# Kernel optimization log

Measured on AMD Instinct MI355X. Metric: run time of the kernel, lower is better.

## Reference

```python
import jax, jax.numpy as jnp
import numpy as np

N_NODES = 20000
N_EDGES = 320000
N_GRAPHS = 100
NEG_SLOPE = 0.2  # DGL GATConv default


def _gat_layer(x, src, dst, W, al, ar, b):
    # x: [N, Din]; W: [Din, H*D]; al, ar: [H, D]; b: [H*D]
    H, D = al.shape
    N = x.shape[0]
    f = (x @ W).reshape(N, H, D)                      # projected feats [N,H,D]
    el = (f * al[None]).sum(-1)                       # [N,H]
    er = (f * ar[None]).sum(-1)                       # [N,H]
    e = jax.nn.leaky_relu(el[src] + er[dst], NEG_SLOPE)  # [E,H] edge logits
    m = jax.ops.segment_max(e, dst, num_segments=N)   # per-dst max for stability
    m = jnp.where(jnp.isfinite(m), m, 0.0)            # zero-in-degree safety
    ex = jnp.exp(e - m[dst])                          # [E,H]
    s = jax.ops.segment_sum(ex, dst, num_segments=N)  # [N,H]
    a = ex / s[dst]                                   # edge softmax
    msg = f[src] * a[:, :, None]                      # [E,H,D]
    out = jax.ops.segment_sum(msg, dst, num_segments=N)  # [N,H,D]
    return out + b.reshape(1, H, D)


def setup_inputs() -> dict:
    key = jax.random.key(0)
    ks = jax.random.split(key, 16)
    x = jax.random.normal(ks[0], (N_NODES, 64), jnp.float32)
    src = jax.random.randint(ks[1], (N_EDGES,), 0, N_NODES, jnp.int32)
    dst = jax.random.randint(ks[2], (N_EDGES,), 0, N_NODES, jnp.int32)
    graph_id = jnp.sort(jax.random.randint(ks[3], (N_NODES,), 0, N_GRAPHS, jnp.int32))
    sc = lambda k, s: jax.random.normal(k, s, jnp.float32) * (1.0 / np.sqrt(s[0]))
    return {
        'x': x, 'src': src, 'dst': dst, 'graph_id': graph_id,
        'W1': sc(ks[4], (64, 640)), 'al1': jax.random.normal(ks[5], (10, 64)) * 0.1,
        'ar1': jax.random.normal(ks[6], (10, 64)) * 0.1, 'b1': jnp.zeros((640,), jnp.float32),
        'W2': sc(ks[7], (64, 128)), 'al2': jax.random.normal(ks[8], (1, 128)) * 0.1,
        'ar2': jax.random.normal(ks[9], (1, 128)) * 0.1, 'b2': jnp.zeros((128,), jnp.float32),
        'lw1': sc(ks[10], (128, 128)), 'lb1': jnp.zeros((128,), jnp.float32),
        'lw2': sc(ks[11], (128, 1)), 'lb2': jnp.zeros((1,), jnp.float32),
    }


def reference(x, src, dst, graph_id, W1, al1, ar1, b1, W2, al2, ar2, b2, lw1, lb1, lw2, lb2):
    h = jax.nn.relu(_gat_layer(x, src, dst, W1, al1, ar1, b1))   # [N,10,64]
    h = h.sum(axis=1)                                            # [N,64]
    h = jax.nn.relu(_gat_layer(h, src, dst, W2, al2, ar2, b2))   # [N,1,128]
    g = jax.ops.segment_max(h, graph_id, num_segments=N_GRAPHS)  # [B,1,128] max readout
    g = jnp.where(jnp.isfinite(g), g, 0.0)                       # empty-graph safety
    g = jax.nn.relu(g @ lw1 + lb1)                               # [B,1,128]
    g = jax.nn.relu(g @ lw2 + lb2)                               # [B,1,1]
    return g.reshape(-1)                                         # [B]
```

## Files before the change

### kernel.cpp

```cpp
#include <hip/hip_runtime.h>
#include <hip/hip_fp16.h>
#include <math.h>

typedef _Float16 half8 __attribute__((ext_vector_type(8)));
typedef float floatx4 __attribute__((ext_vector_type(4)));

__device__ __forceinline__ float leaky(float v){ return v > 0.f ? v : 0.2f*v; }

__device__ __forceinline__ float wredsum(float v){
  #pragma unroll
  for (int o=32;o>0;o>>=1) v += __shfl_xor(v,o,64);
  return v;
}

__device__ __forceinline__ unsigned fkey(float f){
  unsigned b = __float_as_uint(f);
  return (b & 0x80000000u) ? ~b : (b | 0x80000000u);
}
__device__ __forceinline__ float funkey(unsigned u){
  unsigned b = (u & 0x80000000u) ? (u ^ 0x80000000u) : ~u;
  return __uint_as_float(b);
}
#define KEY_NEGINF 0x007FFFFFu

__global__ void k_prep(const float* __restrict__ x, const float* __restrict__ W1,
                       const float* __restrict__ W2,
                       const float* __restrict__ al1, const float* __restrict__ ar1,
                       const float* __restrict__ al2, const float* __restrict__ ar2,
                       __half* __restrict__ xh, __half* __restrict__ w1t, __half* __restrict__ w2t,
                       float* __restrict__ qal1, float* __restrict__ qar1,
                       float* __restrict__ qal2, float* __restrict__ qar2,
                       int* __restrict__ deg, int* __restrict__ gbuf, int N, int ngbuf){
  int i = blockIdx.x*blockDim.x + threadIdx.x;
  if (i < N){ deg[i] = 0; return; }
  i -= N;
  if (i < ngbuf){ gbuf[i] = 0; return; }
  i -= ngbuf;
  const int nx = N*64;
  if (i < nx){ xh[i] = __float2half(x[i]); return; }
  i -= nx;
  if (i < 640*64){ int c = i >> 6, k = i & 63; w1t[i] = __float2half(W1[k*640 + c]); return; }
  i -= 640*64;
  if (i < 128*64){ int c = i >> 6, k = i & 63; w2t[i] = __float2half(W2[k*128 + c]); return; }
  i -= 128*64;
  if (i < 1280){
    int which = i / 640; int j = i - which*640; int k = j / 10, h = j - k*10;
    const float* av = which ? ar1 : al1;
    float s = 0.f;
    for (int c=0;c<64;c++) s += W1[k*640 + h*64 + c] * av[h*64 + c];
    (which ? qar1 : qal1)[k*10 + h] = s;
    return;
  }
  i -= 1280;
  if (i < 128){
    int which = i >> 6; int k = i & 63;
    const float* av = which ? ar2 : al2;
    float s = 0.f;
    for (int c=0;c<128;c++) s += W2[k*128 + c] * av[c];
    (which ? qar2 : qal2)[k] = s;
    return;
  }
}

__global__ __launch_bounds__(256) void k_coef_hist(const float* __restrict__ x,
                                                   const float* __restrict__ qal, const float* __restrict__ qar,
                                                   float* __restrict__ el, float* __restrict__ er,
                                                   unsigned* __restrict__ pmx, int N, int gxCoef,
                                                   const int* __restrict__ dst, int* __restrict__ deg, int E){
  __shared__ float xs[64][65];
  __shared__ float qs[64][20];
  __shared__ unsigned smx[20];
  const int t = threadIdx.x;
  if (blockIdx.x >= gxCoef){
    int i = (blockIdx.x - gxCoef)*256 + t;
    if (i < E) atomicAdd(&deg[dst[i]], 1);
    return;
  }
  const int base = blockIdx.x*64;
  if (t < 20) smx[t] = KEY_NEGINF;
  for (int idx = t; idx < 1280; idx += 256){
    int k = idx/20, j = idx - k*20;
    qs[k][j] = (j < 10) ? qal[k*10 + j] : qar[k*10 + (j-10)];
  }
  #pragma unroll
  for (int q=0;q<16;q++){
    int idx = t + q*256;
    int r = idx>>6, c = idx&63;
    xs[r][c] = (base + r < N) ? x[(size_t)(base+r)*64 + c] : 0.f;
  }
  __syncthreads();
  const int nl = t & 63;
  const int g  = t >> 6;
  const int n  = base + nl;
  float p[5] = {0,0,0,0,0};
  #pragma unroll 8
  for (int k=0;k<64;k++){
    float xv = xs[nl][k];
    #pragma unroll
    for (int j5=0;j5<5;j5++) p[j5] += xv * qs[k][g*5+j5];
  }
  if (n < N){
    #pragma unroll
    for (int j5=0;j5<5;j5++){
      int j = g*5 + j5;
      if (j < 10) el[(size_t)n*10 + j] = p[j5];
      else        er[(size_t)n*10 + (j-10)] = p[j5];
      atomicMax(&smx[j], fkey(p[j5]));
    }
  }
  __syncthreads();
  if (t < 20) pmx[(size_t)blockIdx.x*20 + t] = smx[t];
}

__global__ __launch_bounds__(1024) void k_scan(const int* __restrict__ deg, int* __restrict__ off,
                                               int* __restrict__ cur, int N,
                                               const unsigned* __restrict__ pmx,
                                               unsigned* __restrict__ gmx, int nblk){
  __shared__ unsigned smx[20];
  __shared__ int wsum[16];
  const int t = threadIdx.x;
  const int wid = t >> 6, lane = t & 63;
  if (t < 20) smx[t] = KEY_NEGINF;
  __syncthreads();
  if (t < 640){
    int j = t % 20, b0 = t / 20;
    unsigned m = KEY_NEGINF;
    for (int b = b0; b < nblk; b += 32) m = max(m, pmx[(size_t)b*20 + j]);
    atomicMax(&smx[j], m);
  }
  __syncthreads();
  if (t < 20) gmx[t] = smx[t];
  int carry = 0;
  const int ntile = (N + 1023) >> 10;
  for (int tile = 0; tile < ntile; ++tile){
    const int idx = (tile << 10) + t;
    const int v = (idx < N) ? deg[idx] : 0;
    int sc = v;
    #pragma unroll
    for (int o=1;o<64;o<<=1){
      int u = __shfl_up(sc, o, 64);
      if (lane >= o) sc += u;
    }
    if (lane == 63) wsum[wid] = sc;
    __syncthreads();
    if (t < 16){
      int wv = wsum[t];
      #pragma unroll
      for (int o=1;o<16;o<<=1){
        int u = __shfl_up(wv, o, 64);
        if (t >= o) wv += u;
      }
      wsum[t] = wv;
    }
    __syncthreads();
    const int waveBase = (wid > 0) ? wsum[wid-1] : 0;
    const int ex = carry + waveBase + sc - v;
    if (idx < N){ off[idx] = ex; cur[idx] = ex; }
    carry += wsum[15];
    __syncthreads();
  }
  if (t == 0) off[N] = carry;
}

__global__ void k_scatw(const int* __restrict__ src, const int* __restrict__ dst,
                        int* __restrict__ cur, const float* __restrict__ el,
                        const float* __restrict__ er, const unsigned* __restrict__ gmx,
                        int* __restrict__ srcs, __half* __restrict__ aw16, int E){
  int i = blockIdx.x*blockDim.x + threadIdx.x;
  if (i >= E) return;
  int s0 = src[i], d0 = dst[i];
  int p = atomicAdd(&cur[d0], 1);
  srcs[p] = s0;
  const float* elp = el + (size_t)s0*10;
  const float* erp = er + (size_t)d0*10;
  union { _Float16 h[16]; uint4 u[2]; } w;
  #pragma unroll
  for (int h=0;h<10;h++){
    float m = leaky(funkey(gmx[h]) + funkey(gmx[10+h]));
    w.h[h] = (_Float16)__expf(leaky(elp[h] + erp[h]) - m);
  }
  #pragma unroll
  for (int h=10;h<16;h++) w.h[h] = (_Float16)0.f;
  uint4* o = reinterpret_cast<uint4*>(aw16 + (size_t)p*16);
  o[0] = w.u[0];
  o[1] = w.u[1];
}

__global__ __launch_bounds__(64) void k_edge1(const __half* __restrict__ xh,
                                              const __half* __restrict__ aw16,
                                              const int* __restrict__ off,
                                              const int* __restrict__ srcs,
                                              __half* __restrict__ aggh, int N){
  const int l = threadIdx.x;
  const int n = blockIdx.x;
  const int lr = l & 15, lk = l >> 4;
  const int beg = off[n], end = off[n+1];
  float s = 0.f;
  floatx4 acc0 = {0.f,0.f,0.f,0.f}, acc1 = {0.f,0.f,0.f,0.f};
  floatx4 acc2 = {0.f,0.f,0.f,0.f}, acc3 = {0.f,0.f,0.f,0.f};
  for (int c0 = beg; c0 < end; c0 += 32){
    int sv = (c0 + l < end) ? srcs[c0 + l] : 0;
    int sj[8];
    #pragma unroll
    for (int j=0;j<8;j++) sj[j] = __shfl(sv, lk*8 + j, 64);
    half8 aw;
    #pragma unroll
    for (int j=0;j<8;j++){
      int p = c0 + lk*8 + j;
      _Float16 wv = (_Float16)0.f;
      if (p < end) wv = *(const _Float16*)(aw16 + (size_t)p*16 + lr);
      aw[j] = wv;
      s += (float)wv;
    }
    half8 b0, b1, b2, b3;
    #pragma unroll
    for (int j=0;j<8;j++){
      const __half* rp = xh + (size_t)sj[j]*64;
      b0[j] = *(const _Float16*)(rp + lr);
      b1[j] = *(const _Float16*)(rp + 16 + lr);
      b2[j] = *(const _Float16*)(rp + 32 + lr);
      b3[j] = *(const _Float16*)(rp + 48 + lr);
    }
    acc0 = __builtin_amdgcn_mfma_f32_16x16x32_f16(aw, b0, acc0, 0, 0, 0);
    acc1 = __builtin_amdgcn_mfma_f32_16x16x32_f16(aw, b1, acc1, 0, 0, 0);
    acc2 = __builtin_amdgcn_mfma_f32_16x16x32_f16(aw, b2, acc2, 0, 0, 0);
    acc3 = __builtin_amdgcn_mfma_f32_16x16x32_f16(aw, b3, acc3, 0, 0, 0);
  }
  s += __shfl_xor(s,16,64);
  s += __shfl_xor(s,32,64);
  const float rs = (lr < 10 && s > 0.f) ? 1.f/s : 0.f;
  #pragma unroll
  for (int j=0;j<4;j++){
    int h = lk*4 + j;
    float rj = __shfl(rs, h, 64);
    if (h < 10){
      __half* op = aggh + (size_t)n*640 + h*64;
      op[lr]      = __float2half(acc0[j] * rj);
      op[16 + lr] = __float2half(acc1[j] * rj);
      op[32 + lr] = __float2half(acc2[j] * rj);
      op[48 + lr] = __float2half(acc3[j] * rj);
    }
  }
}

__global__ __launch_bounds__(256) void k_ep1(const __half* __restrict__ aggh,
                                             const __half* __restrict__ w1t,
                                             const float* __restrict__ bias1,
                                             __half* __restrict__ h1h,
                                             const float* __restrict__ qal2,
                                             const float* __restrict__ qar2,
                                             float* __restrict__ el2, float* __restrict__ er2, int M){
  const int w = threadIdx.x >> 6, l = threadIdx.x & 63;
  const int m0 = blockIdx.x*64 + w*16;
  const int lr = l & 15, lk = l >> 4;
  int arow = m0 + lr; if (arow >= M) arow = M-1;
  float hsum[4][4];
  #pragma unroll
  for (int t=0;t<4;t++)
    #pragma unroll
    for (int j=0;j<4;j++) hsum[t][j] = 0.f;
  for (int h=0;h<10;h++){
    const __half* ap = aggh + (size_t)arow*640 + h*64;
    half8 a0 = *reinterpret_cast<const half8*>(ap + lk*8);
    half8 a1 = *reinterpret_cast<const half8*>(ap + 32 + lk*8);
    #pragma unroll
    for (int t=0;t<4;t++){
      const __half* bp = w1t + (size_t)(h*64 + t*16 + lr)*64 + lk*8;
      half8 b0 = *reinterpret_cast<const half8*>(bp);
      half8 b1 = *reinterpret_cast<const half8*>(bp + 32);
      floatx4 z = {0.f,0.f,0.f,0.f};
      z = __builtin_amdgcn_mfma_f32_16x16x32_f16(a0, b0, z, 0, 0, 0);
      z = __builtin_amdgcn_mfma_f32_16x16x32_f16(a1, b1, z, 0, 0, 0);
      float bb = bias1[h*64 + t*16 + lr];
      #pragma unroll
      for (int j=0;j<4;j++) hsum[t][j] += fmaxf(z[j] + bb, 0.f);
    }
  }
  #pragma unroll
  for (int t=0;t<4;t++)
    #pragma unroll
    for (int j=0;j<4;j++){
      int r = m0 + lk*4 + j;
      if (r < M) h1h[(size_t)r*64 + t*16 + lr] = __float2half(hsum[t][j]);
    }
  float pl[4] = {0,0,0,0}, pr[4] = {0,0,0,0};
  #pragma unroll
  for (int t=0;t<4;t++){
    float qa = qal2[t*16 + lr];
    float qr = qar2[t*16 + lr];
    #pragma unroll
    for (int j=0;j<4;j++){ pl[j] += hsum[t][j]*qa; pr[j] += hsum[t][j]*qr; }
  }
  #pragma unroll
  for (int o=1;o<16;o<<=1)
    #pragma unroll
    for (int j=0;j<4;j++){ pl[j] += __shfl_xor(pl[j],o,64); pr[j] += __shfl_xor(pr[j],o,64); }
  if (lr == 0){
    #pragma unroll
    for (int j=0;j<4;j++){
      int r = m0 + lk*4 + j;
      if (r < M){ el2[r] = pl[j]; er2[r] = pr[j]; }
    }
  }
}

__global__ __launch_bounds__(256) void k_edge2(const __half* __restrict__ h1h,
                                               const float* __restrict__ el2,
                                               const float* __restrict__ er,
                                               const int* __restrict__ off,
                                               const int* __restrict__ srcs,
                                               __half* __restrict__ agg2h, int N){
  const int lane = threadIdx.x & 63;
  const int n = blockIdx.x*4 + (threadIdx.x >> 6);
  if (n >= N) return;
  const int beg = off[n], end = off[n+1];
  const float ern = er[n];
  float s = 0.f, acc = 0.f;
  for (int c0 = beg; c0 < end; c0 += 64){
    const bool vl = (c0 + lane < end);
    const int sv = vl ? srcs[c0 + lane] : 0;
    const float gv = vl ? el2[sv] : -INFINITY;
    const float wv = __expf(leaky(gv + ern));
    s += wv;
    const int cn = min(64, end - c0);
    for (int j = 0; j < cn; j += 8){
      const int nv = min(8, cn - j);
      float hv[8], wj[8];
      #pragma unroll
      for (int jj=0;jj<8;jj++){
        if (jj < nv){
          int sj = __shfl(sv, j+jj, 64);
          hv[jj] = __half2float(h1h[(size_t)sj*64 + lane]);
          wj[jj] = __shfl(wv, j+jj, 64);
        }
      }
      #pragma unroll
      for (int jj=0;jj<8;jj++) if (jj < nv) acc += wj[jj]*hv[jj];
    }
  }
  s = wredsum(s);
  const float rs = (s > 0.f) ? 1.f/s : 0.f;
  agg2h[(size_t)n*64 + lane] = __float2half(acc * rs);
}

__global__ __launch_bounds__(256) void k_l2g(const __half* __restrict__ ah,
                                             const __half* __restrict__ wt,
                                             const float* __restrict__ bias2,
                                             const int* __restrict__ gid,
                                             int* __restrict__ gbuf, int M){
  __shared__ float hs[64][65];
  const int w = threadIdx.x >> 6, l = threadIdx.x & 63;
  const int base = blockIdx.x*64;
  const int m0 = base + w*16;
  const int c0 = blockIdx.y*64;
  const int lr = l & 15, lk = l >> 4;
  int arow = m0 + lr; if (arow >= M) arow = M-1;
  half8 a0 = *reinterpret_cast<const half8*>(ah + (size_t)arow*64 + lk*8);
  half8 a1 = *reinterpret_cast<const half8*>(ah + (size_t)arow*64 + 32 + lk*8);
  #pragma unroll
  for (int t=0;t<4;t++){
    const __half* bp = wt + (size_t)(c0 + t*16 + lr)*64 + lk*8;
    half8 b0 = *reinterpret_cast<const half8*>(bp);
    half8 b1 = *reinterpret_cast<const half8*>(bp + 32);
    floatx4 z = {0.f,0.f,0.f,0.f};
    z = __builtin_amdgcn_mfma_f32_16x16x32_f16(a0, b0, z, 0, 0, 0);
    z = __builtin_amdgcn_mfma_f32_16x16x32_f16(a1, b1, z, 0, 0, 0);
    float bb = bias2[c0 + t*16 + lr];
    #pragma unroll
    for (int j=0;j<4;j++)
      hs[w*16 + lk*4 + j][t*16 + lr] = fmaxf(z[j] + bb, 0.f);
  }
  __syncthreads();
  const int col = threadIdx.x & 63;
  const int rg  = threadIdx.x >> 6;
  int curg = -1; float mx = 0.f;
  for (int r = rg*16; r < rg*16 + 16; ++r){
    int gr = base + r;
    if (gr >= M) break;
    int gg = gid[gr];
    if (gg != curg){
      if (curg >= 0) atomicMax(&gbuf[curg*128 + c0 + col], __float_as_int(mx));
      curg = gg; mx = 0.f;
    }
    mx = fmaxf(mx, hs[r][col]);
  }
  if (curg >= 0) atomicMax(&gbuf[curg*128 + c0 + col], __float_as_int(mx));
}

__global__ __launch_bounds__(128) void k_mlp(const int* __restrict__ g,
                                             const float* __restrict__ lw1, const float* __restrict__ lb1,
                                             const float* __restrict__ lw2, const float* __restrict__ lb2,
                                             float* __restrict__ out){
  int b = blockIdx.x, t = threadIdx.x;
  __shared__ float gs[128];
  __shared__ float ys[128];
  gs[t] = __int_as_float(g[b*128 + t]);
  __syncthreads();
  float y = lb1[t];
  for (int k=0;k<128;k++) y += gs[k]*lw1[k*128 + t];
  y = fmaxf(y, 0.f);
  ys[t] = y * lw2[t];
  __syncthreads();
  for (int o=64;o>0;o>>=1){
    if (t < o) ys[t] += ys[t+o];
    __syncthreads();
  }
  if (t == 0) out[b] = fmaxf(ys[0] + lb2[0], 0.f);
}

extern "C" void kernel_launch(void* const* d_in, const int* in_sizes, int n_in,
                              void* d_out, int out_size, void* d_ws, size_t ws_size,
                              hipStream_t stream){
  const float* x   = (const float*)d_in[0];
  const int*   src = (const int*)d_in[1];
  const int*   dst = (const int*)d_in[2];
  const int*   gid = (const int*)d_in[3];
  const float* W1  = (const float*)d_in[4];
  const float* al1 = (const float*)d_in[5];
  const float* ar1 = (const float*)d_in[6];
  const float* b1  = (const float*)d_in[7];
  const float* W2  = (const float*)d_in[8];
  const float* al2 = (const float*)d_in[9];
  const float* ar2 = (const float*)d_in[10];
  const float* b2  = (const float*)d_in[11];
  const float* lw1 = (const float*)d_in[12];
  const float* lb1 = (const float*)d_in[13];
  const float* lw2 = (const float*)d_in[14];
  const float* lb2 = (const float*)d_in[15];
  float* out = (float*)d_out;

  const int N = in_sizes[0] / 64;
  const int E = in_sizes[1];
  const int G = out_size;

  char* w = (char*)d_ws;
  size_t p = 0;
  auto alloc = [&](size_t bytes)->char*{ char* r = w + p; p += (bytes + 255) & ~size_t(255); return r; };
  int*      deg   = (int*)alloc((size_t)N*4);
  int*      off   = (int*)alloc((size_t)(N+1)*4);
  int*      cur   = (int*)alloc((size_t)N*4);
  int*      srcs  = (int*)alloc((size_t)E*4);
  float*    el1   = (float*)alloc((size_t)N*10*4);
  float*    er1   = (float*)alloc((size_t)N*10*4);
  unsigned* gmx   = (unsigned*)alloc(20*4);
  __half*   aw16  = (__half*)alloc((size_t)E*16*2);
  __half*   xh    = (__half*)alloc((size_t)N*64*2);
  __half*   w1t   = (__half*)alloc((size_t)640*64*2);
  __half*   w2t   = (__half*)alloc((size_t)128*64*2);
  float*    qal1  = (float*)alloc((size_t)640*4);
  float*    qar1  = (float*)alloc((size_t)640*4);
  float*    qal2  = (float*)alloc((size_t)64*4);
  float*    qar2  = (float*)alloc((size_t)64*4);
  __half*   aggh  = (__half*)alloc((size_t)N*640*2);
  __half*   h1h   = (__half*)alloc((size_t)N*64*2);
  __half*   agg2h = (__half*)alloc((size_t)N*64*2);
  int*      gbuf  = (int*)alloc((size_t)G*128*4);
  const int gx  = (N + 63) / 64;
  unsigned* pmx   = (unsigned*)alloc((size_t)gx*20*4);
  float*    el2 = el1;
  float*    er2 = er1;

  const int prep_total = N + G*128 + N*64 + 640*64 + 128*64 + 1280 + 128;
  const int histBlocks = (E + 255) / 256;

  k_prep     <<<dim3((prep_total+255)/256), dim3(256), 0, stream>>>(x, W1, W2, al1, ar1, al2, ar2,
                                                                    xh, w1t, w2t, qal1, qar1, qal2, qar2,
                                                                    deg, gbuf, N, G*128);
  k_coef_hist<<<dim3(gx + histBlocks), dim3(256), 0, stream>>>(x, qal1, qar1, el1, er1, pmx, N, gx,
                                                               dst, deg, E);
  k_scan     <<<dim3(1), dim3(1024), 0, stream>>>(deg, off, cur, N, pmx, gmx, gx);
  k_scatw    <<<dim3(histBlocks), dim3(256), 0, stream>>>(src, dst, cur, el1, er1, gmx, srcs, aw16, E);

  k_edge1    <<<dim3(N), dim3(64), 0, stream>>>(xh, aw16, off, srcs, aggh, N);
  k_ep1      <<<dim3(gx), dim3(256), 0, stream>>>(aggh, w1t, b1, h1h, qal2, qar2, el2, er2, N);

  k_edge2    <<<dim3((N+3)/4), dim3(256), 0, stream>>>(h1h, el2, er2, off, srcs, agg2h, N);
  k_l2g      <<<dim3(gx, 2), dim3(256), 0, stream>>>(agg2h, w2t, b2, gid, gbuf, N);

  k_mlp      <<<dim3(G), dim3(128), 0, stream>>>(gbuf, lw1, lb1, lw2, lb2, out);
}
```

Baseline: 163.6 us.

## Stage gathered source rows in swizzled LDS with vector loads in edge1

The first-layer aggregation kernel now gathers each 32-edge chunk of source feature rows and attention weights with 16-byte coalesced global loads into per-wave shared memory. It uses an XOR swizzle to avoid bank conflicts, then builds the MFMA operands from LDS. Before, each lane made scattered 2-byte global loads. Four destination nodes share one 256-thread block instead of one 64-thread block per node. The added LDS traffic and the explicit lgkmcnt wait add some latency per chunk. The code relies on in-wave lockstep and has no barrier.

```diff
diff --git a/kernel.cpp b/kernel.cpp
--- a/kernel.cpp
+++ b/kernel.cpp
@@ -186,40 +186,57 @@
   o[1] = w.u[1];
 }
 
-__global__ __launch_bounds__(64) void k_edge1(const __half* __restrict__ xh,
-                                              const __half* __restrict__ aw16,
-                                              const int* __restrict__ off,
-                                              const int* __restrict__ srcs,
-                                              __half* __restrict__ aggh, int N){
-  const int l = threadIdx.x;
-  const int n = blockIdx.x;
+__global__ __launch_bounds__(256) void k_edge1(const __half* __restrict__ xh,
+                                               const __half* __restrict__ aw16,
+                                               const int* __restrict__ off,
+                                               const int* __restrict__ srcs,
+                                               __half* __restrict__ aggh, int N){
+  __shared__ __align__(16) _Float16 bsm[4][32][64];
+  __shared__ __align__(16) _Float16 asm_[4][32][16];
+  const int wid = threadIdx.x >> 6;
+  const int l   = threadIdx.x & 63;
+  const int n = blockIdx.x*4 + wid;
+  if (n >= N) return;
   const int lr = l & 15, lk = l >> 4;
   const int beg = off[n], end = off[n+1];
+  _Float16 (*bw)[64] = bsm[wid];
+  _Float16 (*aswp)[16] = asm_[wid];
   float s = 0.f;
   floatx4 acc0 = {0.f,0.f,0.f,0.f}, acc1 = {0.f,0.f,0.f,0.f};
   floatx4 acc2 = {0.f,0.f,0.f,0.f}, acc3 = {0.f,0.f,0.f,0.f};
   for (int c0 = beg; c0 < end; c0 += 32){
-    int sv = (c0 + l < end) ? srcs[c0 + l] : 0;
-    int sj[8];
-    #pragma unroll
-    for (int j=0;j<8;j++) sj[j] = __shfl(sv, lk*8 + j, 64);
-    half8 aw;
+    const int sv = (c0 + l < end) ? srcs[c0 + l] : 0;
+    {
+      int e = l >> 1, part = l & 1;
+      int p = c0 + e;
+      uint4 v = make_uint4(0,0,0,0);
+      if (p < end) v = *reinterpret_cast<const uint4*>(aw16 + (size_t)p*16 + part*8);
+      *reinterpret_cast<uint4*>(&aswp[e][part*8]) = v;
+    }
+    #pragma unroll
+    for (int q=0;q<4;q++){
+      int linear = q*64 + l;
+      int row = linear >> 3;
+      int c8  = linear & 7;
+      int rn  = __shfl(sv, row, 64);
+      uint4 v = *reinterpret_cast<const uint4*>(xh + (size_t)rn*64 + c8*8);
+      int gw = c8 ^ (row >> 3);
+      *reinterpret_cast<uint4*>(&bw[row][gw*8]) = v;
+    }
+    asm volatile("s_waitcnt lgkmcnt(0)" ::: "memory");
+    half8 aw, b0, b1, b2, b3;
     #pragma unroll
     for (int j=0;j<8;j++){
-      int p = c0 + lk*8 + j;
-      _Float16 wv = (_Float16)0.f;
-      if (p < end) wv = *(const _Float16*)(aw16 + (size_t)p*16 + lr);
-      aw[j] = wv;
-      s += (float)wv;
-    }
-    half8 b0, b1, b2, b3;
-    #pragma unroll
-    for (int j=0;j<8;j++){
-      const __half* rp = xh + (size_t)sj[j]*64;
-      b0[j] = *(const _Float16*)(rp + lr);
-      b1[j] = *(const _Float16*)(rp + 16 + lr);
-      b2[j] = *(const _Float16*)(rp + 32 + lr);
-      b3[j] = *(const _Float16*)(rp + 48 + lr);
+      const int row = lk*8 + j;
+      const int sw  = lk;
+      const int hi  = lr >> 3;
+      const int e0  = lr & 7;
+      aw[j] = aswp[row][lr];
+      s += (float)aw[j];
+      b0[j] = bw[row][((hi    ) ^ sw)*8 + e0];
+      b1[j] = bw[row][((2 + hi) ^ sw)*8 + e0];
+      b2[j] = bw[row][((4 + hi) ^ sw)*8 + e0];
+      b3[j] = bw[row][((6 + hi) ^ sw)*8 + e0];
     }
     acc0 = __builtin_amdgcn_mfma_f32_16x16x32_f16(aw, b0, acc0, 0, 0, 0);
     acc1 = __builtin_amdgcn_mfma_f32_16x16x32_f16(aw, b1, acc1, 0, 0, 0);
@@ -471,7 +488,7 @@
   k_scan     <<<dim3(1), dim3(1024), 0, stream>>>(deg, off, cur, N, pmx, gmx, gx);
   k_scatw    <<<dim3(histBlocks), dim3(256), 0, stream>>>(src, dst, cur, el1, er1, gmx, srcs, aw16, E);
 
-  k_edge1    <<<dim3(N), dim3(64), 0, stream>>>(xh, aw16, off, srcs, aggh, N);
+  k_edge1    <<<dim3((N+3)/4), dim3(256), 0, stream>>>(xh, aw16, off, srcs, aggh, N);
   k_ep1      <<<dim3(gx), dim3(256), 0, stream>>>(aggh, w1t, b1, h1h, qal2, qar2, el2, er2, N);
 
   k_edge2    <<<dim3((N+3)/4), dim3(256), 0, stream>>>(h1h, el2, er2, off, srcs, agg2h, N);
```

Result: no change. 165.6 us (+1.3%).
